# Performance work log

Hardware: AMD Instinct MI355X
Metric: run time of the kernel (lower is better)

## Reference

```python
import jax, jax.numpy as jnp
import numpy as np

B, S = 1, 2048
HID, NH, NKV, HD = 2048, 16, 4, 128
NREP = NH // NKV  # 4
WIN = 1024
ROPE_THETA = 10000.0


def rotate_half(t):
    t1, t2 = jnp.split(t, 2, axis=-1)
    return jnp.concatenate([-t2, t1], axis=-1)


def setup_inputs() -> dict:
    key = jax.random.key(0)
    ks = jax.random.split(key, 5)
    x = jax.random.normal(ks[0], (B, S, HID), dtype=jnp.float32)
    # causal sliding-window additive mask: 0 where attended, -1e9 elsewhere
    i = jnp.arange(S)
    allowed = (i[None, :] <= i[:, None]) & (i[:, None] - i[None, :] < WIN)
    attention_mask = jnp.where(allowed, 0.0, -1e9).astype(jnp.float32)[None, None]  # [1,1,S,S]
    wq = jax.random.normal(ks[1], (NH * HD, HID), dtype=jnp.float32) * 0.02
    wk = jax.random.normal(ks[2], (NKV * HD, HID), dtype=jnp.float32) * 0.02
    wv = jax.random.normal(ks[3], (NKV * HD, HID), dtype=jnp.float32) * 0.02
    wo = jax.random.normal(ks[4], (HID, NH * HD), dtype=jnp.float32) * 0.02
    return {"x": x, "attention_mask": attention_mask, "wq": wq, "wk": wk, "wv": wv, "wo": wo}


def reference(x, attention_mask, wq, wk, wv, wo):
    b, s, _ = x.shape
    q = (x @ wq.T).reshape(b, s, NH, HD)
    k = (x @ wk.T).reshape(b, s, NKV, HD)
    v = (x @ wv.T).reshape(b, s, NKV, HD)
    # rotary embeddings (HF-style rotate_half)
    inv_freq = 1.0 / (ROPE_THETA ** (jnp.arange(0, HD, 2, dtype=jnp.float32) / HD))
    freqs = jnp.arange(s, dtype=jnp.float32)[:, None] * inv_freq[None, :]  # [s, HD/2]
    emb = jnp.concatenate([freqs, freqs], axis=-1)  # [s, HD]
    cos = jnp.cos(emb)[None, :, None, :]
    sin = jnp.sin(emb)[None, :, None, :]
    q = q * cos + rotate_half(q) * sin
    k = k * cos + rotate_half(k) * sin
    # GQA: repeat kv heads
    k = jnp.repeat(k, NREP, axis=2)  # [b, s, NH, HD]
    v = jnp.repeat(v, NREP, axis=2)
    scores = jnp.einsum('bqhd,bkhd->bhqk', q, k) / jnp.sqrt(jnp.float32(HD)) + attention_mask
    probs = jax.nn.softmax(scores.astype(jnp.float32), axis=-1).astype(q.dtype)
    out = jnp.einsum('bhqk,bkhd->bqhd', probs, v).reshape(b, s, NH * HD)
    return out @ wo.T
```

## Files before the change

### kernel.cpp

```cpp
#include <hip/hip_runtime.h>


#define AS1 __attribute__((address_space(1)))
#define AS3 __attribute__((address_space(3)))

typedef short v8s __attribute__((ext_vector_type(8)));
typedef short v4s __attribute__((ext_vector_type(4)));
typedef float v4f __attribute__((ext_vector_type(4)));

__device__ __forceinline__ void gload16(const void* g, void* l) {
  __builtin_amdgcn_global_load_lds((AS1 void*)g, (AS3 void*)l, 16, 0, 0);
}

__device__ __forceinline__ short f2bf(float f) {
  union { float f; unsigned u; } v; v.f = f;
  unsigned r = (v.u + 0x7FFFu + ((v.u >> 16) & 1u)) >> 16;
  return (short)r;
}
__device__ __forceinline__ float bf2f(short h) {
  union { unsigned u; float f; } v; v.u = ((unsigned)(unsigned short)h) << 16;
  return v.f;
}
__device__ __forceinline__ bool sniff_bf16(const unsigned* mask) {
  return mask[1] == 0xCE6ECE6Eu;
}

__device__ __forceinline__ int colmap(int w, int nt, int r) {
  return (w & 1) * 32 + (nt & 1) * 16 + (nt >> 1) * 64 + r;
}

#define ROPE_L2T (13.287712379549449f / 64.0f)
#define Q_SCALE  (1.4426950408889634f * 0.08838834764831845f)

template <bool BF> struct Raw8;
template <> struct Raw8<true>  { v8s v; };
template <> struct Raw8<false> { float4 a, b; };

template <bool BF> __device__ __forceinline__ Raw8<BF> ldraw(const void* p, size_t e);
template <> __device__ __forceinline__ Raw8<true> ldraw<true>(const void* p, size_t e) {
  Raw8<true> r; r.v = *(const v8s*)((const short*)p + e); return r;
}
template <> __device__ __forceinline__ Raw8<false> ldraw<false>(const void* p, size_t e) {
  Raw8<false> r; const float* f = (const float*)p + e;
  r.a = *(const float4*)f; r.b = *(const float4*)(f + 4); return r;
}
template <bool BF> __device__ __forceinline__ v8s cvt8(const Raw8<BF>& r);
template <> __device__ __forceinline__ v8s cvt8<true>(const Raw8<true>& r) { return r.v; }
template <> __device__ __forceinline__ v8s cvt8<false>(const Raw8<false>& r) {
  v8s o;
  o[0] = f2bf(r.a.x); o[1] = f2bf(r.a.y); o[2] = f2bf(r.a.z); o[3] = f2bf(r.a.w);
  o[4] = f2bf(r.b.x); o[5] = f2bf(r.b.y); o[6] = f2bf(r.b.z); o[7] = f2bf(r.b.w);
  return o;
}

__global__ __launch_bounds__(256) void convert_kernel(
    const void* __restrict__ X, const void* __restrict__ WQ,
    const void* __restrict__ WK, const void* __restrict__ WV,
    const void* __restrict__ WO, const unsigned* __restrict__ mask,
    short* __restrict__ Xbf, short* __restrict__ Wqkvbf, short* __restrict__ WObf)
{
  const bool bf = sniff_bf16(mask);
  size_t e = ((size_t)blockIdx.x * 256 + threadIdx.x) * 8;
  const void* src; short* dst; size_t off, doff;
  if (e < 4194304)       { src = X;  dst = Xbf;  off = e; doff = e; }
  else if (e < 10485760) {
    size_t wv = e - 4194304; dst = Wqkvbf; doff = wv;
    if (wv < 4194304)      { src = WQ; off = wv; }
    else if (wv < 5242880) { src = WK; off = wv - 4194304; }
    else                   { src = WV; off = wv - 5242880; }
  }
  else                   { src = WO; dst = WObf; off = e - 10485760; doff = off; }
  v8s v = bf ? ldraw<true>(src, off).v : cvt8<false>(ldraw<false>(src, off));
  *(v8s*)&dst[doff] = v;
}

__device__ __forceinline__ void gemm_dma_loop(
    const short* __restrict__ A, const short* __restrict__ Bt,
    int m0, int brow0, short* lA, short* lB, v4f acc[2][4])
{
  const int tid = threadIdx.x;
  const int w = tid >> 6, lane = tid & 63;
  const int quad = lane >> 4, r = lane & 15;
  const int wm = (w >> 1) * 32;
  const int rlo = lane >> 2, c8 = (lane & 3) * 8;

  size_t ga[2]; short* la[2];
#pragma unroll
  for (int j = 0; j < 2; ++j) {
    int cA = w * 2 + j;
    int p = cA >> 2, local = cA & 3;
    ga[j] = (size_t)(m0 + local * 16 + rlo) * 2048 + p * 32 + c8;
    la[j] = lA + cA * 512;
  }
  size_t gb[4]; short* lb[4];
#pragma unroll
  for (int j = 0; j < 4; ++j) {
    int cB = w * 4 + j;
    int p = cB >> 3, local = cB & 7;
    gb[j] = (size_t)(brow0 + local * 16 + rlo) * 2048 + p * 32 + c8;
    lb[j] = lB + cB * 512;
  }

  for (int k0 = 0; k0 < 2048; k0 += 64) {
    if (k0) __syncthreads();
#pragma unroll
    for (int j = 0; j < 2; ++j) gload16(A + ga[j] + k0, la[j]);
#pragma unroll
    for (int j = 0; j < 4; ++j) gload16(Bt + gb[j] + k0, lb[j]);
    __syncthreads();
#pragma unroll
    for (int ks = 0; ks < 2; ++ks) {
      v8s a[2], b[4];
#pragma unroll
      for (int mt = 0; mt < 2; ++mt)
        a[mt] = *(const v8s*)&lA[ks * 2048 + (wm + mt * 16 + r) * 32 + quad * 8];
#pragma unroll
      for (int nt = 0; nt < 4; ++nt)
        b[nt] = *(const v8s*)&lB[ks * 4096 + colmap(w, nt, r) * 32 + quad * 8];
#pragma unroll
      for (int mt = 0; mt < 2; ++mt)
#pragma unroll
        for (int nt = 0; nt < 4; ++nt)
          acc[mt][nt] = __builtin_amdgcn_mfma_f32_16x16x32_bf16(a[mt], b[nt], acc[mt][nt], 0, 0, 0);
    }
  }
}

__device__ __forceinline__ void qkv_epilogue(
    v4f acc[2][4], int m0, int n0, short* Qo, short* Ko, short* VTo)
{
  const int tid = threadIdx.x;
  const int w = tid >> 6, lane = tid & 63;
  const int quad = lane >> 4, r = lane & 15;
  const int wm = (w >> 1) * 32;
  const int rowb = m0 + wm + quad * 4;

  if (n0 < 2560) {
    const bool isQ = (n0 < 2048);
    short* dst = isQ ? Qo : Ko;
    const int ld = isQ ? 2048 : 512;
    const int base = isQ ? n0 : (n0 - 2048);
    const float sc = isQ ? Q_SCALE : 1.0f;
#pragma unroll
    for (int nt = 0; nt < 2; ++nt) {
      int d = (w & 1) * 32 + nt * 16 + r;
      float inv = exp2f(-(float)d * ROPE_L2T);
#pragma unroll
      for (int mt = 0; mt < 2; ++mt)
#pragma unroll
        for (int i = 0; i < 4; ++i) {
          int row = rowb + mt * 16 + i;
          float ang = (float)row * inv;
          float cs = cosf(ang), sn = sinf(ang);
          float x1 = acc[mt][nt][i], x2 = acc[mt][nt + 2][i];
          dst[(size_t)row * ld + base + d]      = f2bf((x1 * cs - x2 * sn) * sc);
          dst[(size_t)row * ld + base + d + 64] = f2bf((x2 * cs + x1 * sn) * sc);
        }
    }
  } else {
#pragma unroll
    for (int mt = 0; mt < 2; ++mt)
#pragma unroll
      for (int nt = 0; nt < 4; ++nt) {
        int row = rowb + mt * 16;
        int vcol = n0 - 2560 + colmap(w, nt, r);
        v4s pk;
#pragma unroll
        for (int i = 0; i < 4; ++i) pk[i] = f2bf(acc[mt][nt][i]);
        *(v4s*)&VTo[(size_t)vcol * 2048 + row] = pk;
      }
  }
}

__global__ __launch_bounds__(256, 3) void gemm_qkv_dma(
    const short* __restrict__ Xbf, const short* __restrict__ Wqkvbf,
    short* __restrict__ Qo, short* __restrict__ Ko, short* __restrict__ VTo)
{
  __shared__ __align__(16) short lA[64 * 64];
  __shared__ __align__(16) short lB[128 * 64];
  const int m0 = blockIdx.x * 64;
  const int n0 = blockIdx.y * 128;
  v4f acc[2][4];
#pragma unroll
  for (int i = 0; i < 2; ++i)
#pragma unroll
    for (int j = 0; j < 4; ++j) acc[i][j] = v4f{0.f, 0.f, 0.f, 0.f};
  gemm_dma_loop(Xbf, Wqkvbf, m0, n0, lA, lB, acc);
  qkv_epilogue(acc, m0, n0, Qo, Ko, VTo);
}

__global__ __launch_bounds__(256, 3) void gemm_out_dma(
    const short* __restrict__ A, const short* __restrict__ WObf,
    const unsigned* __restrict__ mask, void* __restrict__ Out)
{
  __shared__ __align__(16) short lA[64 * 64];
  __shared__ __align__(16) short lB[128 * 64];
  const int m0 = blockIdx.x * 64;
  const int n0 = blockIdx.y * 128;
  v4f acc[2][4];
#pragma unroll
  for (int i = 0; i < 2; ++i)
#pragma unroll
    for (int j = 0; j < 4; ++j) acc[i][j] = v4f{0.f, 0.f, 0.f, 0.f};
  gemm_dma_loop(A, WObf, m0, n0, lA, lB, acc);

  const bool bf = sniff_bf16(mask);
  const int tid = threadIdx.x;
  const int w = tid >> 6, lane = tid & 63;
  const int quad = lane >> 4, r = lane & 15;
  const int wm = (w >> 1) * 32;
  const int rowb = m0 + wm + quad * 4;
#pragma unroll
  for (int mt = 0; mt < 2; ++mt)
#pragma unroll
    for (int nt = 0; nt < 4; ++nt) {
      int row = rowb + mt * 16;
      int col = n0 + colmap(w, nt, r);
#pragma unroll
      for (int i = 0; i < 4; ++i) {
        size_t idx = (size_t)(row + i) * 2048 + col;
        if (bf) ((short*)Out)[idx] = f2bf(acc[mt][nt][i]);
        else    ((float*)Out)[idx] = acc[mt][nt][i];
      }
    }
}

template <bool BFA, bool BFB>
__device__ __forceinline__ void gemm64x128_loop(
    const void* __restrict__ A, const void* __restrict__ Bt,
    int m0, int brow0, short* lA, short* lB, v4f acc[2][4])
{
  const int tid = threadIdx.x;
  const int w = tid >> 6, lane = tid & 63;
  const int quad = lane >> 4, r = lane & 15;
  const int wm = (w >> 1) * 32;

  int uoffA[2]; size_t ea[2];
#pragma unroll
  for (int j = 0; j < 2; ++j) {
    int u = tid + 256 * j;
    int row = u >> 3, c = (u & 7) * 8;
    uoffA[j] = (c & 32) * 64 + row * 32 + (c & 31);
    ea[j] = (size_t)(m0 + row) * 2048 + c;
  }
  int uoffB[4]; size_t eb[4];
#pragma unroll
  for (int j = 0; j < 4; ++j) {
    int u = tid + 256 * j;
    int row = u >> 3, c = (u & 7) * 8;
    uoffB[j] = (c & 32) * 128 + row * 32 + (c & 31);
    eb[j] = (size_t)(brow0 + row) * 2048 + c;
  }

  for (int k0 = 0; k0 < 2048; k0 += 64) {
    Raw8<BFA> ta[2]; Raw8<BFB> tb[4];
#pragma unroll
    for (int j = 0; j < 2; ++j) ta[j] = ldraw<BFA>(A, ea[j] + k0);
#pragma unroll
    for (int j = 0; j < 4; ++j) tb[j] = ldraw<BFB>(Bt, eb[j] + k0);
    if (k0) __syncthreads();
#pragma unroll
    for (int j = 0; j < 2; ++j) *(v8s*)&lA[uoffA[j]] = cvt8<BFA>(ta[j]);
#pragma unroll
    for (int j = 0; j < 4; ++j) *(v8s*)&lB[uoffB[j]] = cvt8<BFB>(tb[j]);
    __syncthreads();
#pragma unroll
    for (int ks = 0; ks < 2; ++ks) {
      v8s a[2], b[4];
#pragma unroll
      for (int mt = 0; mt < 2; ++mt)
        a[mt] = *(const v8s*)&lA[ks * 2048 + (wm + mt * 16 + r) * 32 + quad * 8];
#pragma unroll
      for (int nt = 0; nt < 4; ++nt)
        b[nt] = *(const v8s*)&lB[ks * 4096 + colmap(w, nt, r) * 32 + quad * 8];
#pragma unroll
      for (int mt = 0; mt < 2; ++mt)
#pragma unroll
        for (int nt = 0; nt < 4; ++nt)
          acc[mt][nt] = __builtin_amdgcn_mfma_f32_16x16x32_bf16(a[mt], b[nt], acc[mt][nt], 0, 0, 0);
    }
  }
}

__global__ __launch_bounds__(256, 3) void gemm_qkv_fb(
    const void* __restrict__ X, const void* __restrict__ WQ,
    const void* __restrict__ WK, const void* __restrict__ WV,
    const unsigned* __restrict__ mask,
    short* __restrict__ Qo, short* __restrict__ Ko, short* __restrict__ VTo)
{
  __shared__ __align__(16) short lA[64 * 64];
  __shared__ __align__(16) short lB[128 * 64];
  const int m0 = blockIdx.x * 64;
  const int n0 = blockIdx.y * 128;
  const void* Bt; int brow0;
  if (n0 < 2048)      { Bt = WQ; brow0 = n0; }
  else if (n0 < 2560) { Bt = WK; brow0 = n0 - 2048; }
  else                { Bt = WV; brow0 = n0 - 2560; }

  v4f acc[2][4];
#pragma unroll
  for (int i = 0; i < 2; ++i)
#pragma unroll
    for (int j = 0; j < 4; ++j) acc[i][j] = v4f{0.f, 0.f, 0.f, 0.f};

  if (sniff_bf16(mask)) gemm64x128_loop<true, true>(X, Bt, m0, brow0, lA, lB, acc);
  else                  gemm64x128_loop<false, false>(X, Bt, m0, brow0, lA, lB, acc);
  qkv_epilogue(acc, m0, n0, Qo, Ko, VTo);
}

__global__ __launch_bounds__(256, 3) void gemm_out_fb(
    const short* __restrict__ A, const void* __restrict__ WO,
    const unsigned* __restrict__ mask, void* __restrict__ Out)
{
  __shared__ __align__(16) short lA[64 * 64];
  __shared__ __align__(16) short lB[128 * 64];
  const bool bf = sniff_bf16(mask);
  const int m0 = blockIdx.x * 64;
  const int n0 = blockIdx.y * 128;

  v4f acc[2][4];
#pragma unroll
  for (int i = 0; i < 2; ++i)
#pragma unroll
    for (int j = 0; j < 4; ++j) acc[i][j] = v4f{0.f, 0.f, 0.f, 0.f};

  if (bf) gemm64x128_loop<true, true>(A, WO, m0, n0, lA, lB, acc);
  else    gemm64x128_loop<true, false>(A, WO, m0, n0, lA, lB, acc);

  const int tid = threadIdx.x;
  const int w = tid >> 6, lane = tid & 63;
  const int quad = lane >> 4, r = lane & 15;
  const int wm = (w >> 1) * 32;
  const int rowb = m0 + wm + quad * 4;
#pragma unroll
  for (int mt = 0; mt < 2; ++mt)
#pragma unroll
    for (int nt = 0; nt < 4; ++nt) {
      int row = rowb + mt * 16;
      int col = n0 + colmap(w, nt, r);
#pragma unroll
      for (int i = 0; i < 4; ++i) {
        size_t idx = (size_t)(row + i) * 2048 + col;
        if (bf) ((short*)Out)[idx] = f2bf(acc[mt][nt][i]);
        else    ((float*)Out)[idx] = acc[mt][nt][i];
      }
    }
}

__global__ __launch_bounds__(256, 1) void attn_kernel(
    const short* __restrict__ Q, const short* __restrict__ Kb,
    const short* __restrict__ VT, short* __restrict__ Ao)
{
  __shared__ __align__(16) short lK[64 * 128];
  __shared__ __align__(16) short lV[128 * 64];
  __shared__ __align__(16) short lP[4][16 * 72];

  const int bx = blockIdx.x;
  const int qb = bx >> 4, h = bx & 15;
  const int hk = h >> 2;
  const int q0 = qb * 64;
  const int tid = threadIdx.x, w = tid >> 6, lane = tid & 63;
  const int quad = lane >> 4, r = lane & 15;
  const int wq0 = q0 + w * 16;
  short* lPw = lP[w];

  v8s qa[4];
#pragma unroll
  for (int ks = 0; ks < 4; ++ks)
    qa[ks] = *(const v8s*)(Q + (size_t)(wq0 + r) * 2048 + h * 128 + ks * 32 + quad * 8);

  v4f Oa[8];
#pragma unroll
  for (int dt = 0; dt < 8; ++dt) Oa[dt] = v4f{0.f, 0.f, 0.f, 0.f};
  const float NEG = -3.0e38f;
  float m_i[4], l_i[4];
#pragma unroll
  for (int i = 0; i < 4; ++i) { m_i[i] = NEG; l_i[i] = 0.f; }

  const int t0 = (q0 >= 1024) ? ((q0 - 1023) >> 6) : 0;
  const int t1 = qb;

  for (int t = t0; t <= t1; ++t) {
    const int key0 = t << 6;
    v8s tK[4], tV[4];
#pragma unroll
    for (int u = 0; u < 4; ++u) {
      int lin = (w * 4 + u) * 64 + lane;
      int krow = lin >> 4, kcc = lin & 15;
      tK[u] = *(const v8s*)(Kb + (size_t)(key0 + krow) * 512 + hk * 128 + ((kcc ^ krow) & 15) * 8);
      int vrow = lin >> 3, vcc = lin & 7;
      tV[u] = *(const v8s*)(VT + (size_t)(hk * 128 + vrow) * 2048 + key0 + ((vcc ^ vrow) & 7) * 8);
    }
    if (t > t0) __syncthreads();
#pragma unroll
    for (int u = 0; u < 4; ++u) {
      int lin = (w * 4 + u) * 64 + lane;
      *(v8s*)&lK[lin * 8] = tK[u];
      *(v8s*)&lV[lin * 8] = tV[u];
    }
    __syncthreads();

    v4f s4[4];
#pragma unroll
    for (int nt = 0; nt < 4; ++nt) s4[nt] = v4f{0.f, 0.f, 0.f, 0.f};
#pragma unroll
    for (int ks = 0; ks < 4; ++ks)
#pragma unroll
      for (int nt = 0; nt < 4; ++nt) {
        v8s bk = *(const v8s*)&lK[(nt * 16 + r) * 128 + (((ks * 4 + quad) ^ r) & 15) * 8];
        s4[nt] = __builtin_amdgcn_mfma_f32_16x16x32_bf16(qa[ks], bk, s4[nt], 0, 0, 0);
      }

    const bool full = (key0 + 63 <= wq0) && (wq0 + 15 - key0 < 1024);

    float rowmax[4] = {NEG, NEG, NEG, NEG};
    if (full) {
#pragma unroll
      for (int nt = 0; nt < 4; ++nt)
#pragma unroll
        for (int i = 0; i < 4; ++i) rowmax[i] = fmaxf(rowmax[i], s4[nt][i]);
    } else {
#pragma unroll
      for (int nt = 0; nt < 4; ++nt) {
        int key = key0 + nt * 16 + r;
#pragma unroll
        for (int i = 0; i < 4; ++i) {
          int q = wq0 + quad * 4 + i;
          bool ok = (key <= q) && (q - key < 1024);
          if (ok) rowmax[i] = fmaxf(rowmax[i], s4[nt][i]);
        }
      }
    }
#pragma unroll
    for (int i = 0; i < 4; ++i)
#pragma unroll
      for (int off = 1; off < 16; off <<= 1)
        rowmax[i] = fmaxf(rowmax[i], __shfl_xor(rowmax[i], off, 64));
    float alpha[4], rsum[4] = {0.f, 0.f, 0.f, 0.f};
#pragma unroll
    for (int i = 0; i < 4; ++i) {
      float mn = fmaxf(m_i[i], rowmax[i]);
      alpha[i] = exp2f(m_i[i] - mn);
      m_i[i] = mn;
    }
    if (full) {
#pragma unroll
      for (int nt = 0; nt < 4; ++nt)
#pragma unroll
        for (int i = 0; i < 4; ++i) {
          float p = exp2f(s4[nt][i] - m_i[i]);
          rsum[i] += p;
          lPw[(quad * 4 + i) * 72 + nt * 16 + r] = f2bf(p);
        }
    } else {
#pragma unroll
      for (int nt = 0; nt < 4; ++nt) {
        int key = key0 + nt * 16 + r;
#pragma unroll
        for (int i = 0; i < 4; ++i) {
          int q = wq0 + quad * 4 + i;
          bool ok = (key <= q) && (q - key < 1024);
          float p = ok ? exp2f(s4[nt][i] - m_i[i]) : 0.0f;
          rsum[i] += p;
          lPw[(quad * 4 + i) * 72 + nt * 16 + r] = f2bf(p);
        }
      }
    }
#pragma unroll
    for (int i = 0; i < 4; ++i) {
#pragma unroll
      for (int off = 1; off < 16; off <<= 1)
        rsum[i] += __shfl_xor(rsum[i], off, 64);
      l_i[i] = l_i[i] * alpha[i] + rsum[i];
    }
#pragma unroll
    for (int dt = 0; dt < 8; ++dt)
#pragma unroll
      for (int i = 0; i < 4; ++i) Oa[dt][i] *= alpha[i];

#pragma unroll
    for (int ks2 = 0; ks2 < 2; ++ks2) {
      v8s ap = *(const v8s*)&lPw[r * 72 + ks2 * 32 + quad * 8];
#pragma unroll
      for (int dt = 0; dt < 8; ++dt) {
        v8s bv = *(const v8s*)&lV[(dt * 16 + r) * 64 + (((ks2 * 4 + quad) ^ r) & 7) * 8];
        Oa[dt] = __builtin_amdgcn_mfma_f32_16x16x32_bf16(ap, bv, Oa[dt], 0, 0, 0);
      }
    }
  }

  float invl[4];
#pragma unroll
  for (int i = 0; i < 4; ++i) invl[i] = (l_i[i] > 0.f) ? 1.0f / l_i[i] : 0.f;
#pragma unroll
  for (int dt = 0; dt < 8; ++dt)
#pragma unroll
    for (int i = 0; i < 4; ++i) {
      int q = wq0 + quad * 4 + i;
      Ao[(size_t)q * 2048 + h * 128 + dt * 16 + r] = f2bf(Oa[dt][i] * invl[i]);
    }
}

extern "C" void kernel_launch(void* const* d_in, const int* in_sizes, int n_in,
                              void* d_out, int out_size, void* d_ws, size_t ws_size,
                              hipStream_t stream) {
  const void*     x    = d_in[0];
  const unsigned* mask = (const unsigned*)d_in[1];
  const void*     wq   = d_in[2];
  const void*     wk   = d_in[3];
  const void*     wv   = d_in[4];
  const void*     wo   = d_in[5];

  short* Q  = (short*)d_out;
  short* Kb = (short*)d_ws;
  short* VT = Kb + (size_t)1048576;
  short* Ao = VT + (size_t)1048576;

  const size_t NEED = 41943040ull;
  if (ws_size >= NEED) {
    short* Xbf    = Ao + (size_t)4194304;
    short* Wqkvbf = Xbf + (size_t)4194304;
    short* WObf   = Wqkvbf + (size_t)6291456;
    convert_kernel<<<7168, 256, 0, stream>>>(x, wq, wk, wv, wo, mask, Xbf, Wqkvbf, WObf);
    gemm_qkv_dma<<<dim3(32, 24), 256, 0, stream>>>(Xbf, Wqkvbf, Q, Kb, VT);
    attn_kernel<<<512, 256, 0, stream>>>(Q, Kb, VT, Ao);
    gemm_out_dma<<<dim3(32, 16), 256, 0, stream>>>(Ao, WObf, mask, d_out);
  } else {
    gemm_qkv_fb<<<dim3(32, 24), 256, 0, stream>>>(x, wq, wk, wv, mask, Q, Kb, VT);
    attn_kernel<<<512, 256, 0, stream>>>(Q, Kb, VT, Ao);
    gemm_out_fb<<<dim3(32, 16), 256, 0, stream>>>(Ao, wo, mask, d_out);
  }
}
```

Baseline: 227.7 us.

## Use lazy softmax rescaling and compute row sums with an MFMA against ones

```diff
diff --git a/kernel.cpp b/kernel.cpp
--- a/kernel.cpp
+++ b/kernel.cpp
@@ -369,13 +369,18 @@
   for (int ks = 0; ks < 4; ++ks)
     qa[ks] = *(const v8s*)(Q + (size_t)(wq0 + r) * 2048 + h * 128 + ks * 32 + quad * 8);
 
+  v8s ones;
+#pragma unroll
+  for (int j = 0; j < 8; ++j) ones[j] = (short)0x3F80;
+
   v4f Oa[8];
 #pragma unroll
   for (int dt = 0; dt < 8; ++dt) Oa[dt] = v4f{0.f, 0.f, 0.f, 0.f};
+  v4f La = v4f{0.f, 0.f, 0.f, 0.f};
   const float NEG = -3.0e38f;
-  float m_i[4], l_i[4];
-#pragma unroll
-  for (int i = 0; i < 4; ++i) { m_i[i] = NEG; l_i[i] = 0.f; }
+  float m_i[4];
+#pragma unroll
+  for (int i = 0; i < 4; ++i) m_i[i] = NEG;
 
   const int t0 = (q0 >= 1024) ? ((q0 - 1023) >> 6) : 0;
   const int t1 = qb;
@@ -413,12 +418,53 @@
 
     const bool full = (key0 + 63 <= wq0) && (wq0 + 15 - key0 < 1024);
 
-    float rowmax[4] = {NEG, NEG, NEG, NEG};
+    float pm[4];
+#pragma unroll
+    for (int i = 0; i < 4; ++i)
+      pm[i] = fmaxf(fmaxf(s4[0][i], s4[1][i]), fmaxf(s4[2][i], s4[3][i]));
+    bool grow = false;
+#pragma unroll
+    for (int i = 0; i < 4; ++i) grow |= (pm[i] > m_i[i] + 8.f);
+
+    if (__any((int)grow)) {
+      float rowmax[4] = {NEG, NEG, NEG, NEG};
+      if (full) {
+#pragma unroll
+        for (int i = 0; i < 4; ++i) rowmax[i] = pm[i];
+      } else {
+#pragma unroll
+        for (int nt = 0; nt < 4; ++nt) {
+          int key = key0 + nt * 16 + r;
+#pragma unroll
+          for (int i = 0; i < 4; ++i) {
+            int q = wq0 + quad * 4 + i;
+            bool ok = (key <= q) && (q - key < 1024);
+            if (ok) rowmax[i] = fmaxf(rowmax[i], s4[nt][i]);
+          }
+        }
+      }
+#pragma unroll
+      for (int i = 0; i < 4; ++i)
+#pragma unroll
+        for (int off = 1; off < 16; off <<= 1)
+          rowmax[i] = fmaxf(rowmax[i], __shfl_xor(rowmax[i], off, 64));
+#pragma unroll
+      for (int i = 0; i < 4; ++i) {
+        float mn = fmaxf(m_i[i], rowmax[i]);
+        float al = exp2f(m_i[i] - mn);
+        m_i[i] = mn;
+        La[i] *= al;
+#pragma unroll
+        for (int dt = 0; dt < 8; ++dt) Oa[dt][i] *= al;
+      }
+    }
+
     if (full) {
 #pragma unroll
       for (int nt = 0; nt < 4; ++nt)
 #pragma unroll
-        for (int i = 0; i < 4; ++i) rowmax[i] = fmaxf(rowmax[i], s4[nt][i]);
+        for (int i = 0; i < 4; ++i)
+          lPw[(quad * 4 + i) * 72 + nt * 16 + r] = f2bf(exp2f(s4[nt][i] - m_i[i]));
     } else {
 #pragma unroll
       for (int nt = 0; nt < 4; ++nt) {
@@ -427,60 +473,16 @@
         for (int i = 0; i < 4; ++i) {
           int q = wq0 + quad * 4 + i;
           bool ok = (key <= q) && (q - key < 1024);
-          if (ok) rowmax[i] = fmaxf(rowmax[i], s4[nt][i]);
+          lPw[(quad * 4 + i) * 72 + nt * 16 + r] =
+              ok ? f2bf(exp2f(s4[nt][i] - m_i[i])) : (short)0;
         }
       }
     }
-#pragma unroll
-    for (int i = 0; i < 4; ++i)
-#pragma unroll
-      for (int off = 1; off < 16; off <<= 1)
-        rowmax[i] = fmaxf(rowmax[i], __shfl_xor(rowmax[i], off, 64));
-    float alpha[4], rsum[4] = {0.f, 0.f, 0.f, 0.f};
-#pragma unroll
-    for (int i = 0; i < 4; ++i) {
-      float mn = fmaxf(m_i[i], rowmax[i]);
-      alpha[i] = exp2f(m_i[i] - mn);
-      m_i[i] = mn;
-    }
-    if (full) {
-#pragma unroll
-      for (int nt = 0; nt < 4; ++nt)
-#pragma unroll
-        for (int i = 0; i < 4; ++i) {
-          float p = exp2f(s4[nt][i] - m_i[i]);
-          rsum[i] += p;
-          lPw[(quad * 4 + i) * 72 + nt * 16 + r] = f2bf(p);
-        }
-    } else {
-#pragma unroll
-      for (int nt = 0; nt < 4; ++nt) {
-        int key = key0 + nt * 16 + r;
-#pragma unroll
-        for (int i = 0; i < 4; ++i) {
-          int q = wq0 + quad * 4 + i;
-          bool ok = (key <= q) && (q - key < 1024);
-          float p = ok ? exp2f(s4[nt][i] - m_i[i]) : 0.0f;
-          rsum[i] += p;
-          lPw[(quad * 4 + i) * 72 + nt * 16 + r] = f2bf(p);
-        }
-      }
-    }
-#pragma unroll
-    for (int i = 0; i < 4; ++i) {
-#pragma unroll
-      for (int off = 1; off < 16; off <<= 1)
-        rsum[i] += __shfl_xor(rsum[i], off, 64);
-      l_i[i] = l_i[i] * alpha[i] + rsum[i];
-    }
-#pragma unroll
-    for (int dt = 0; dt < 8; ++dt)
-#pragma unroll
-      for (int i = 0; i < 4; ++i) Oa[dt][i] *= alpha[i];
 
 #pragma unroll
     for (int ks2 = 0; ks2 < 2; ++ks2) {
       v8s ap = *(const v8s*)&lPw[r * 72 + ks2 * 32 + quad * 8];
+      La = __builtin_amdgcn_mfma_f32_16x16x32_bf16(ap, ones, La, 0, 0, 0);
 #pragma unroll
       for (int dt = 0; dt < 8; ++dt) {
         v8s bv = *(const v8s*)&lV[(dt * 16 + r) * 64 + (((ks2 * 4 + quad) ^ r) & 7) * 8];
@@ -491,7 +493,7 @@
 
   float invl[4];
 #pragma unroll
-  for (int i = 0; i < 4; ++i) invl[i] = (l_i[i] > 0.f) ? 1.0f / l_i[i] : 0.f;
+  for (int i = 0; i < 4; ++i) invl[i] = (La[i] > 0.f) ? 1.0f / La[i] : 0.f;
 #pragma unroll
   for (int dt = 0; dt < 8; ++dt)
 #pragma unroll
```

New measurement: 217.5 us. -4.5%, faster.
